# Performance work log

Measured on AMD Instinct MI355X. Metric: run time of the kernel, lower is better.

## Reference

```python
import jax, jax.numpy as jnp
import numpy as np

B, T1, T2, C, H, NIN = 4, 4096, 2048, 512, 8, 3
D = C // H  # head_dim = 64


def setup_inputs() -> dict:
    key = jax.random.key(0)
    ks = jax.random.split(key, 10)
    s = 0.02  # weight init scale
    return {
        "x": jax.random.normal(ks[0], (B, T1, C), jnp.float32),
        "y0": jax.random.normal(ks[1], (B, T2, C), jnp.float32),
        "y1": jax.random.normal(ks[2], (B, T2, C), jnp.float32),
        "y2": jax.random.normal(ks[3], (B, T2, C), jnp.float32),
        "Wq": jax.random.normal(ks[4], (C, C), jnp.float32) * s,
        "bq": jnp.zeros((C,), jnp.float32),
        "Wk": jax.random.normal(ks[5], (NIN, C, C), jnp.float32) * s,
        "bk": jnp.zeros((NIN, C), jnp.float32),
        "Wv": jax.random.normal(ks[6], (NIN, C, C), jnp.float32) * s,
        "bv": jnp.zeros((NIN, C), jnp.float32),
        "Wo": jax.random.normal(ks[7], (C, C), jnp.float32) * s,
        "bo": jnp.zeros((C,), jnp.float32),
    }


def _heads(t, n_head):
    b, n, c = t.shape
    return t.reshape(b, n, n_head, c // n_head).transpose(0, 2, 1, 3)  # [B,H,N,D]


def reference(x, y0, y1, y2, Wq, bq, Wk, bk, Wv, bv, Wo, bo):
    b, t1, c = x.shape
    q = jax.nn.softmax(_heads(x @ Wq.T + bq, H), axis=-1)  # [B,H,T1,D]
    out = q  # note: original initializes accumulator with q itself
    for i, y in enumerate((y0, y1, y2)):
        k = jax.nn.softmax(_heads(y @ Wk[i].T + bk[i], H), axis=-1)  # [B,H,T2,D]
        v = _heads(y @ Wv[i].T + bv[i], H)                            # [B,H,T2,D]
        k_sum = k.sum(axis=-2, keepdims=True)                         # [B,H,1,D]
        D_inv = 1.0 / ((q * k_sum).sum(axis=-1, keepdims=True) + 1e-8)  # [B,H,T1,1]
        context = jnp.einsum('bhnd,bhnv->bhdv', k, v)                 # [B,H,D,D]
        out = out + jnp.einsum('bhqd,bhdv->bhqv', q, context) * D_inv
    out = out.transpose(0, 2, 1, 3).reshape(b, t1, c)
    return out @ Wo.T + bo
```

## Files before the change

### kernel.cpp

```cpp
#include <hip/hip_runtime.h>
#include <stdint.h>

#define B_ 4
#define T1_ 4096
#define T2_ 2048
#define C_ 512
#define H_ 8
#define D_ 64
#define M1_ (B_*T1_)
#define M2_ (B_*T2_)

using f32x4 = __attribute__((ext_vector_type(4))) float;
using bf16x8 = __attribute__((ext_vector_type(8))) __bf16;
using us8 = __attribute__((ext_vector_type(8))) unsigned short;
using us4 = __attribute__((ext_vector_type(4))) unsigned short;

__device__ __forceinline__ unsigned short f2bf(float f){
  unsigned int u = __builtin_bit_cast(unsigned int, f);
  unsigned int r = (u + 0x7fffu + ((u >> 16) & 1u)) >> 16;
  return (unsigned short)r;
}
__device__ __forceinline__ float bf2f(unsigned short u){
  return __builtin_bit_cast(float, ((unsigned int)u) << 16);
}
__device__ __forceinline__ f32x4 mfma16(us8 a, us8 b, f32x4 c){
  return __builtin_amdgcn_mfma_f32_16x16x32_bf16(
      __builtin_bit_cast(bf16x8, a), __builtin_bit_cast(bf16x8, b), c, 0, 0, 0);
}
__device__ __forceinline__ us8 cvt8(f32x4 a, f32x4 b){
  us8 v;
  #pragma unroll
  for (int j = 0; j < 4; ++j){ v[j] = f2bf(a[j]); v[4+j] = f2bf(b[j]); }
  return v;
}

typedef const __attribute__((address_space(1))) unsigned int gu32;
typedef __attribute__((address_space(3))) unsigned int lu32;
__device__ __forceinline__ void gl_lds16(const void* g, void* l){
  __builtin_amdgcn_global_load_lds((gu32*)g, (lu32*)l, 16, 0, 0);
}

#define WAIT_VM(N) asm volatile("s_waitcnt vmcnt(" #N ")" ::: "memory")
#define WAIT_LGKM() asm volatile("s_waitcnt lgkmcnt(0)" ::: "memory")
#define RAW_BAR()  { __builtin_amdgcn_s_barrier(); __builtin_amdgcn_sched_barrier(0); }

__device__ __forceinline__ int swz(int row, int blk){ return blk ^ ((row >> 1) & 3); }

__global__ __launch_bounds__(256) void cvt_bf16_4(const float* __restrict__ p0, const float* __restrict__ p1,
                                                  const float* __restrict__ p2, const float* __restrict__ p3,
                                                  unsigned short* o0, unsigned short* o1,
                                                  unsigned short* o2, unsigned short* o3,
                                                  int n0, int n1, int n2, int n3){
  const float* in; unsigned short* out; int n4;
  switch (blockIdx.y){
    case 0: in = p0; out = o0; n4 = n0; break;
    case 1: in = p1; out = o1; n4 = n1; break;
    case 2: in = p2; out = o2; n4 = n2; break;
    default: in = p3; out = o3; n4 = n3; break;
  }
  int i = blockIdx.x * 256 + threadIdx.x;
  if (i >= n4) return;
  f32x4 v = ((const f32x4*)in)[i];
  us4 o;
  #pragma unroll
  for (int j = 0; j < 4; ++j) o[j] = f2bf(v[j]);
  ((us4*)out)[i] = o;
}

__device__ __forceinline__ void tile_write(unsigned short* tile, const f32x4 (&vals)[4][4],
                                           int wr, int wc, int lr, int lk){
  #pragma unroll
  for (int mt = 0; mt < 4; ++mt)
    #pragma unroll
    for (int nt = 0; nt < 4; ++nt)
      #pragma unroll
      for (int r = 0; r < 4; ++r){
        int row = wr*64 + mt*16 + lk*4 + r;
        int cb  = (wc*128 + nt*32 + lr*2) ^ ((row & 7) << 4);
        *(unsigned short*)((char*)tile + row*256 + cb) = f2bf(vals[mt][nt][r]);
      }
}
__device__ __forceinline__ void tile_write_T(unsigned short* tile, const f32x4 (&vals)[4][4],
                                             int wr, int wc, int lr, int lk){
  #pragma unroll
  for (int mt = 0; mt < 4; ++mt)
    #pragma unroll
    for (int nt = 0; nt < 4; ++nt)
      #pragma unroll
      for (int r = 0; r < 4; ++r){
        int n  = wr*64 + mt*16 + lk*4 + r;
        int ch = wc*64 + nt*16 + lr;
        int cb = (n*2) ^ ((ch & 7) << 4);
        *(unsigned short*)((char*)tile + ch*256 + cb) = f2bf(vals[mt][nt][r]);
      }
}
__device__ __forceinline__ void tile_flush(const unsigned short* tile, unsigned short* g,
                                           size_t row0, int col0, int ldg, int t){
  #pragma unroll
  for (int p = 0; p < 8; ++p){
    int row = p*16 + (t >> 4);
    int cb  = ((t & 15) * 16) ^ ((row & 7) << 4);
    us8 v = *(const us8*)((const char*)tile + row*256 + cb);
    *(us8*)(g + (row0 + row) * (size_t)ldg + col0 + (t & 15) * 8) = v;
  }
}

__global__ __launch_bounds__(256, 3) void proj(const float* __restrict__ xf,
                                               const float* __restrict__ y0f,
                                               const float* __restrict__ y1f,
                                               const float* __restrict__ y2f,
                                               const unsigned short* __restrict__ wqb,
                                               const unsigned short* __restrict__ wkb,
                                               const unsigned short* __restrict__ wvb,
                                               const float* __restrict__ bq,
                                               const float* __restrict__ bk,
                                               const float* __restrict__ bv,
                                               unsigned short* __restrict__ qb,
                                               unsigned short* __restrict__ kbT,
                                               unsigned short* __restrict__ vbT,
                                               float* __restrict__ ksum){
  __shared__ unsigned short smem[20480];
  const int hw = blockIdx.x;
  const int work = (hw & 7) * 256 + (hw >> 3);
  int seg, ii, m0, n0;
  const float* Af;
  const unsigned short* W;
  const float* bias;
  if (work < 512){
    seg = 0; ii = 0;
    m0 = (work >> 2) << 7; n0 = (work & 3) << 7;
    Af = xf; W = wqb; bias = bq;
  } else {
    int r = work - 512;
    int g = r >> 3, s = r & 7;
    ii = g >> 6; m0 = (g & 63) << 7;
    seg = (s < 4) ? 1 : 2;
    n0 = (s & 3) << 7;
    Af = (ii == 0) ? y0f : (ii == 1 ? y1f : y2f);
    W = (seg == 1 ? wkb : wvb) + (size_t)ii*C_*C_;
    bias = (seg == 1 ? bk : bv) + (size_t)ii*C_;
  }
  const int t = threadIdx.x;
  const int w = t >> 6, l = t & 63;
  const int wr = w >> 1, wc = w & 1;
  const int lr = l & 15, lk = l >> 4;
  const int row0 = t >> 2,          b0 = t & 3;
  const int row1 = (t + 256) >> 2,  b1 = t & 3;
  f32x4 acc[4][4] = {};
  f32x4 ar0[4], ar1[4];

#define LOADA(AR, TT) { \
    const float* ap0 = Af + (size_t)(m0+row0)*C_ + (TT)*32 + b0*8; \
    const float* ap1 = Af + (size_t)(m0+row1)*C_ + (TT)*32 + b1*8; \
    AR[0] = *(const f32x4*)ap0; AR[1] = *(const f32x4*)(ap0 + 4); \
    AR[2] = *(const f32x4*)ap1; AR[3] = *(const f32x4*)(ap1 + 4); }
#define DSWA(AR, BUF) { \
    *(us8*)&smem[(BUF)*4096 + row0*32 + swz(row0,b0)*8] = cvt8(AR[0], AR[1]); \
    *(us8*)&smem[(BUF)*4096 + row1*32 + swz(row1,b1)*8] = cvt8(AR[2], AR[3]); }
#define GLW(BUF, TT) { \
    int c=t, row=c>>2; \
    gl_lds16(W + (size_t)(n0+row)*C_ + (TT)*32 + swz(row,c&3)*8, &smem[8192+(BUF)*4096 + c*8]); \
    c=t+256; row=c>>2; \
    gl_lds16(W + (size_t)(n0+row)*C_ + (TT)*32 + swz(row,c&3)*8, &smem[8192+(BUF)*4096 + c*8]); }
#define PCOMP(S, WB) { \
    const unsigned short* sA = &smem[(S)*4096]; \
    const unsigned short* sW = &smem[8192 + (WB)*4096]; \
    us8 af[4], bfr[4]; \
    _Pragma("unroll") \
    for (int mt = 0; mt < 4; ++mt){ int R = wr*64 + mt*16 + lr; af[mt] = *(const us8*)&sA[R*32 + swz(R, lk)*8]; } \
    _Pragma("unroll") \
    for (int nt = 0; nt < 4; ++nt){ int R = wc*64 + nt*16 + lr; bfr[nt] = *(const us8*)&sW[R*32 + swz(R, lk)*8]; } \
    __builtin_amdgcn_s_setprio(1); \
    _Pragma("unroll") \
    for (int mt = 0; mt < 4; ++mt) \
      _Pragma("unroll") \
      for (int nt = 0; nt < 4; ++nt) \
        acc[mt][nt] = mfma16(af[mt], bfr[nt], acc[mt][nt]); \
    __builtin_amdgcn_s_setprio(0); }
#define PSTEP(T, AR, S) { \
    WAIT_VM(6); \
    DSWA(AR, S); \
    if ((T) + 2 < 16) { LOADA(AR, (T)+2); GLW(((T)+2)%3, (T)+2); } \
    WAIT_LGKM(); \
    RAW_BAR(); \
    PCOMP(S, (T)%3); }
#define PSTEPL(T, AR, S) { \
    WAIT_VM(0); \
    DSWA(AR, S); \
    WAIT_LGKM(); \
    RAW_BAR(); \
    PCOMP(S, (T)%3); }

  LOADA(ar0, 0); GLW(0, 0);
  LOADA(ar1, 1); GLW(1, 1);
  PSTEP(0,  ar0, 0) PSTEP(1,  ar1, 1) PSTEP(2,  ar0, 0) PSTEP(3,  ar1, 1)
  PSTEP(4,  ar0, 0) PSTEP(5,  ar1, 1) PSTEP(6,  ar0, 0) PSTEP(7,  ar1, 1)
  PSTEP(8,  ar0, 0) PSTEP(9,  ar1, 1) PSTEP(10, ar0, 0) PSTEP(11, ar1, 1)
  PSTEP(12, ar0, 0) PSTEP(13, ar1, 1) PSTEP(14, ar0, 0) PSTEPL(15, ar1, 1)
#undef LOADA
#undef DSWA
#undef GLW
#undef PCOMP
#undef PSTEP
#undef PSTEPL

  {
    float bc[4];
    #pragma unroll
    for (int nt = 0; nt < 4; ++nt) bc[nt] = bias[n0 + wc*64 + nt*16 + lr];
    #pragma unroll
    for (int mt = 0; mt < 4; ++mt)
      #pragma unroll
      for (int nt = 0; nt < 4; ++nt)
        #pragma unroll
        for (int r = 0; r < 4; ++r) acc[mt][nt][r] += bc[nt];
  }
  if (seg <= 1){
    #pragma unroll
    for (int mt = 0; mt < 4; ++mt)
      #pragma unroll
      for (int r = 0; r < 4; ++r){
        float m = fmaxf(fmaxf(acc[mt][0][r], acc[mt][1][r]), fmaxf(acc[mt][2][r], acc[mt][3][r]));
        #pragma unroll
        for (int s = 1; s < 16; s <<= 1) m = fmaxf(m, __shfl_xor(m, s, 64));
        float sum = 0.f;
        #pragma unroll
        for (int nt = 0; nt < 4; ++nt){
          float e = __expf(acc[mt][nt][r] - m);
          acc[mt][nt][r] = e; sum += e;
        }
        #pragma unroll
        for (int s = 1; s < 16; s <<= 1) sum += __shfl_xor(sum, s, 64);
        float inv = 1.0f / sum;
        #pragma unroll
        for (int nt = 0; nt < 4; ++nt) acc[mt][nt][r] *= inv;
      }
  }
  if (seg == 1){
    const int b = m0 >> 11;
    #pragma unroll
    for (int nt = 0; nt < 4; ++nt){
      float cs = 0.f;
      #pragma unroll
      for (int mt = 0; mt < 4; ++mt)
        #pragma unroll
        for (int r = 0; r < 4; ++r) cs += acc[mt][nt][r];
      cs += __shfl_xor(cs, 16, 64);
      cs += __shfl_xor(cs, 32, 64);
      if (lk == 0)
        atomicAdd(&ksum[((size_t)ii*B_ + b)*C_ + n0 + wc*64 + nt*16 + lr], cs);
    }
  }
  __syncthreads();
  if (seg == 0){
    tile_write(smem, acc, wr, wc, lr, lk);
    __syncthreads();
    tile_flush(smem, qb, m0, n0, C_, t);
  } else {
    tile_write_T(smem, acc, wr, wc, lr, lk);
    __syncthreads();
    const int b = m0 >> 11;
    const int n_base = m0 & 2047;
    unsigned short* gT = (seg == 1 ? kbT : vbT);
    tile_flush(smem, gT, ((size_t)ii*B_ + b)*C_ + n0, n_base, T2_, t);
  }
}

__global__ __launch_bounds__(256) void ctx_mfma(const unsigned short* __restrict__ kbT,
                                                const unsigned short* __restrict__ vbT,
                                                float* __restrict__ part){
  const int bh = blockIdx.x, kc = blockIdx.y, i = blockIdx.z;
  const int b = bh >> 3, h = bh & 7;
  const size_t rowbase = ((size_t)i*B_ + b)*C_ + h*64;
  const unsigned short* kT = kbT + rowbase*T2_;
  const unsigned short* vT = vbT + rowbase*T2_;
  const int t = threadIdx.x;
  const int w = t >> 6, l = t & 63;
  const int qr = w >> 1, qc = w & 1;
  const int lr = l & 15, lk = l >> 4;
  const int n00 = kc * 256;
  f32x4 acc[2][2] = {};
  #pragma unroll
  for (int it = 0; it < 8; ++it){
    const int k0 = n00 + it*32 + lk*8;
    us8 a0 = *(const us8*)(kT + (size_t)(qr*32 +      lr)*T2_ + k0);
    us8 a1 = *(const us8*)(kT + (size_t)(qr*32 + 16 + lr)*T2_ + k0);
    us8 b0 = *(const us8*)(vT + (size_t)(qc*32 +      lr)*T2_ + k0);
    us8 b1 = *(const us8*)(vT + (size_t)(qc*32 + 16 + lr)*T2_ + k0);
    acc[0][0] = mfma16(a0, b0, acc[0][0]);
    acc[0][1] = mfma16(a0, b1, acc[0][1]);
    acc[1][0] = mfma16(a1, b0, acc[1][0]);
    acc[1][1] = mfma16(a1, b1, acc[1][1]);
  }
  float* dst = part + (((size_t)i*8 + kc)*32 + bh)*4096;
  #pragma unroll
  for (int fa = 0; fa < 2; ++fa)
    #pragma unroll
    for (int fb = 0; fb < 2; ++fb){
      int d0 = qr*32 + fa*16 + lk*4;
      int e  = qc*32 + fb*16 + lr;
      *(f32x4*)(dst + e*64 + d0) = acc[fa][fb];
    }
}

__global__ __launch_bounds__(256) void ctx_reduce(const float* __restrict__ part,
                                                  unsigned short* __restrict__ ctxTb){
  const int bh = blockIdx.x, i = blockIdx.y, t = threadIdx.x;
  for (int idx = t; idx < 4096; idx += 256){
    float s = 0.f;
    #pragma unroll
    for (int kc = 0; kc < 8; ++kc)
      s += part[(((size_t)i*8 + kc)*32 + bh)*4096 + idx];
    ctxTb[((size_t)i*32 + bh)*4096 + idx] = f2bf(s);
  }
}

__global__ __launch_bounds__(256) void combine(const unsigned short* __restrict__ qb,
                                               const unsigned short* __restrict__ ctxTb,
                                               const float* __restrict__ ksum,
                                               unsigned short* __restrict__ omid){
  __shared__ unsigned short tile[128*128];
  const int hw = blockIdx.x;
  const int work = (hw & 7) * 64 + (hw >> 3);
  const int m0 = (work & 127) << 7, n0 = (work >> 7) << 7;
  const int t = threadIdx.x;
  const int w = t >> 6, l = t & 63;
  const int wr = w >> 1, wc = w & 1;
  const int lr = l & 15, lk = l >> 4;
  const int b = m0 >> 12;
  const int bh = b*8 + (n0 >> 6) + wc;
  #pragma unroll
  for (int p = 0; p < 8; ++p){
    int idx = p*256 + t;
    int row = idx >> 4, ch = idx & 15;
    gl_lds16(qb + (size_t)(m0+row)*C_ + n0 + (ch ^ (row & 7))*8, &tile[idx*8]);
  }
  WAIT_VM(0);
  __syncthreads();
  us8 afr[4][2];
  #pragma unroll
  for (int mt = 0; mt < 4; ++mt)
    #pragma unroll
    for (int kk = 0; kk < 2; ++kk){
      int row = wr*64 + mt*16 + lr;
      int ch = wc*8 + kk*4 + lk;
      afr[mt][kk] = *(const us8*)((const char*)tile + row*256 + ((ch ^ (row & 7)) << 4));
    }
  f32x4 acc[4][4];
  #pragma unroll
  for (int mt = 0; mt < 4; ++mt)
    #pragma unroll
    for (int nt = 0; nt < 4; ++nt)
      #pragma unroll
      for (int r = 0; r < 4; ++r){
        int row = wr*64 + mt*16 + lk*4 + r;
        int cbyte = wc*128 + nt*32 + lr*2;
        int ch = cbyte >> 4;
        unsigned short v = *(const unsigned short*)((const char*)tile + row*256 +
                            ((ch ^ (row & 7)) << 4) + (cbyte & 15));
        acc[mt][nt][r] = bf2f(v);
      }
  us8 bden[2];
  #pragma unroll
  for (int kk = 0; kk < 2; ++kk){
    us8 tmp = {};
    if (lr < 3){
      const float* kp = ksum + ((size_t)lr*B_ + b)*C_ + n0 + wc*64 + kk*32 + lk*8;
      f32x4 c0 = *(const f32x4*)kp;
      f32x4 c1 = *(const f32x4*)(kp + 4);
      #pragma unroll
      for (int j = 0; j < 4; ++j){ tmp[j] = f2bf(c0[j]); tmp[4+j] = f2bf(c1[j]); }
    }
    bden[kk] = tmp;
  }
  f32x4 den[4] = {};
  #pragma unroll
  for (int mt = 0; mt < 4; ++mt)
    #pragma unroll
    for (int kk = 0; kk < 2; ++kk)
      den[mt] = mfma16(afr[mt][kk], bden[kk], den[mt]);
  #pragma unroll 1
  for (int i = 0; i < 3; ++i){
    f32x4 dinv[4];
    #pragma unroll
    for (int mt = 0; mt < 4; ++mt)
      #pragma unroll
      for (int r = 0; r < 4; ++r)
        dinv[mt][r] = 1.0f / (__shfl(den[mt][r], (l & 48) | i, 64) + 1e-8f);
    #pragma unroll
    for (int nt = 0; nt < 4; ++nt){
      us8 bfr[2];
      #pragma unroll
      for (int kk = 0; kk < 2; ++kk)
        bfr[kk] = *(const us8*)(ctxTb + ((size_t)(i*32 + bh))*4096 + (nt*16 + lr)*64 + kk*32 + lk*8);
      f32x4 p[4] = {};
      #pragma unroll
      for (int mt = 0; mt < 4; ++mt)
        #pragma unroll
        for (int kk = 0; kk < 2; ++kk)
          p[mt] = mfma16(afr[mt][kk], bfr[kk], p[mt]);
      #pragma unroll
      for (int mt = 0; mt < 4; ++mt)
        #pragma unroll
        for (int r = 0; r < 4; ++r)
          acc[mt][nt][r] += p[mt][r] * dinv[mt][r];
    }
  }
  __syncthreads();
  tile_write(tile, acc, wr, wc, lr, lk);
  __syncthreads();
  tile_flush(tile, omid, m0, n0, C_, t);
}

__global__ __launch_bounds__(256, 3) void gemm_bt(const unsigned short* __restrict__ A,
                                                  const unsigned short* __restrict__ Bw,
                                                  const float* __restrict__ bias,
                                                  float* __restrict__ out){
  __shared__ unsigned short smem[3*2*4096];
  const int hw = blockIdx.x;
  const int work = (hw & 7) * 64 + (hw >> 3);
  const int m0 = ((work >> 2) & 127) << 7, n0 = (work & 3) << 7;
  const int t = threadIdx.x;
  const int w = t >> 6, l = t & 63;
  const int wr = w >> 1, wc = w & 1;
  const int lr = l & 15, lk = l >> 4;
  f32x4 acc[4][4] = {};

#define GSTAGE(BB, TT) { \
    int c = t, row = c >> 2; \
    gl_lds16(A  + (size_t)(m0+row)*C_ + (TT)*32 + swz(row, c & 3)*8, &smem[(BB)*8192 + c*8]); \
    gl_lds16(Bw + (size_t)(n0+row)*C_ + (TT)*32 + swz(row, c & 3)*8, &smem[(BB)*8192 + 4096 + c*8]); \
    c = t + 256; row = c >> 2; \
    gl_lds16(A  + (size_t)(m0+row)*C_ + (TT)*32 + swz(row, c & 3)*8, &smem[(BB)*8192 + c*8]); \
    gl_lds16(Bw + (size_t)(n0+row)*C_ + (TT)*32 + swz(row, c & 3)*8, &smem[(BB)*8192 + 4096 + c*8]); }
#define GCOMP(BB) { \
    const unsigned short* sA = &smem[(BB)*8192]; \
    const unsigned short* sB = &smem[(BB)*8192 + 4096]; \
    us8 af[4], bfr[4]; \
    _Pragma("unroll") \
    for (int mt = 0; mt < 4; ++mt){ int R = wr*64 + mt*16 + lr; af[mt] = *(const us8*)&sA[R*32 + swz(R, lk)*8]; } \
    _Pragma("unroll") \
    for (int nt = 0; nt < 4; ++nt){ int R = wc*64 + nt*16 + lr; bfr[nt] = *(const us8*)&sB[R*32 + swz(R, lk)*8]; } \
    __builtin_amdgcn_s_setprio(1); \
    _Pragma("unroll") \
    for (int mt = 0; mt < 4; ++mt) \
      _Pragma("unroll") \
      for (int nt = 0; nt < 4; ++nt) \
        acc[mt][nt] = mfma16(af[mt], bfr[nt], acc[mt][nt]); \
    __builtin_amdgcn_s_setprio(0); }
#define GSTEP(T, N) { \
    if ((T) + 2 < 16) GSTAGE(((T)+2)%3, (T)+2); \
    WAIT_VM(N); \
    RAW_BAR(); \
    GCOMP((T)%3); }

  GSTAGE(0, 0); GSTAGE(1, 1);
  GSTEP(0, 8)  GSTEP(1, 8)  GSTEP(2, 8)  GSTEP(3, 8)
  GSTEP(4, 8)  GSTEP(5, 8)  GSTEP(6, 8)  GSTEP(7, 8)
  GSTEP(8, 8)  GSTEP(9, 8)  GSTEP(10, 8) GSTEP(11, 8)
  GSTEP(12, 8) GSTEP(13, 8) GSTEP(14, 4) GSTEP(15, 0)
#undef GSTAGE
#undef GCOMP
#undef GSTEP

  #pragma unroll
  for (int mt = 0; mt < 4; ++mt)
    #pragma unroll
    for (int nt = 0; nt < 4; ++nt)
      #pragma unroll
      for (int r = 0; r < 4; ++r){
        int row = m0 + wr*64 + mt*16 + lk*4 + r;
        int col = n0 + wc*64 + nt*16 + lr;
        out[(size_t)row*C_ + col] = acc[mt][nt][r] + bias[col];
      }
}

extern "C" void kernel_launch(void* const* d_in, const int* in_sizes, int n_in,
                              void* d_out, int out_size, void* d_ws, size_t ws_size,
                              hipStream_t stream){
  const float* x  = (const float*)d_in[0];
  const float* y0 = (const float*)d_in[1];
  const float* y1 = (const float*)d_in[2];
  const float* y2 = (const float*)d_in[3];
  const float* Wq = (const float*)d_in[4];
  const float* bq = (const float*)d_in[5];
  const float* Wk = (const float*)d_in[6];
  const float* bk = (const float*)d_in[7];
  const float* Wv = (const float*)d_in[8];
  const float* bv = (const float*)d_in[9];
  const float* Wo = (const float*)d_in[10];
  const float* bo = (const float*)d_in[11];

  char* ws = (char*)d_ws;
  size_t off = 0;
  auto alloc = [&](size_t bytes)->char*{
    char* p = ws + off; off += (bytes + 1023) & ~((size_t)1023); return p;
  };
  unsigned short* wqb   = (unsigned short*)alloc((size_t)C_*C_*2);
  unsigned short* wkb   = (unsigned short*)alloc((size_t)3*C_*C_*2);
  unsigned short* wvb   = (unsigned short*)alloc((size_t)3*C_*C_*2);
  unsigned short* wob   = (unsigned short*)alloc((size_t)C_*C_*2);
  unsigned short* qb    = (unsigned short*)alloc((size_t)M1_*C_*2);
  unsigned short* kbT   = (unsigned short*)alloc((size_t)3*B_*C_*T2_*2);
  unsigned short* vbT   = (unsigned short*)alloc((size_t)3*B_*C_*T2_*2);
  float*          ksum  = (float*)alloc((size_t)3*B_*C_*4);
  float*          part  = (float*)alloc((size_t)3*8*32*4096*4);
  unsigned short* ctxTb = (unsigned short*)alloc((size_t)3*32*4096*2);
  unsigned short* omid  = (unsigned short*)alloc((size_t)M1_*C_*2);

  (void)hipMemsetAsync(ksum, 0, (size_t)3*B_*C_*4, stream);

  cvt_bf16_4<<<dim3(3*C_*C_/4/256, 4), 256, 0, stream>>>(
      Wq, Wk, Wv, Wo, wqb, wkb, wvb, wob,
      C_*C_/4, 3*C_*C_/4, 3*C_*C_/4, C_*C_/4);

  proj<<<2048, 256, 0, stream>>>(x, y0, y1, y2, wqb, wkb, wvb, bq, bk, bv, qb, kbT, vbT, ksum);
  ctx_mfma<<<dim3(32, 8, 3), 256, 0, stream>>>(kbT, vbT, part);
  ctx_reduce<<<dim3(32, 3), 256, 0, stream>>>(part, ctxTb);
  combine<<<512, 256, 0, stream>>>(qb, ctxTb, ksum, omid);
  gemm_bt<<<512, 256, 0, stream>>>(omid, wob, bo, (float*)d_out);
}
```

Before: 125.2 us.

## Triple-buffer A tile in proj GEMM and use one barrier per k-step

Restructures the projection GEMM main loop so the A operand (fp32 converted to bf16) is triple-buffered in LDS like W. Each step writes the next A tile and issues the next global loads, then runs the MFMAs on the current stage, with a single barrier at the end of the step instead of a barrier right before compute. The aim is to overlap the LDS stores and global loads with matrix math and to cut barrier stalls. It also replaces the manual bf16 rounding with the native __bf16 conversion. LDS use rises from 40 KB to 48 KB per block, which may affect the 3-blocks-per-CU occupancy target, and the vmcnt bookkeeping is delicate.

```diff
diff --git a/kernel.cpp b/kernel.cpp
--- a/kernel.cpp
+++ b/kernel.cpp
@@ -30,7 +30,10 @@
 __device__ __forceinline__ us8 cvt8(f32x4 a, f32x4 b){
   us8 v;
   #pragma unroll
-  for (int j = 0; j < 4; ++j){ v[j] = f2bf(a[j]); v[4+j] = f2bf(b[j]); }
+  for (int j = 0; j < 4; ++j){
+    v[j]   = __builtin_bit_cast(unsigned short, (__bf16)a[j]);
+    v[4+j] = __builtin_bit_cast(unsigned short, (__bf16)b[j]);
+  }
   return v;
 }
 
@@ -119,7 +122,7 @@
                                                unsigned short* __restrict__ kbT,
                                                unsigned short* __restrict__ vbT,
                                                float* __restrict__ ksum){
-  __shared__ unsigned short smem[20480];
+  __shared__ unsigned short smem[24576];
   const int hw = blockIdx.x;
   const int work = (hw & 7) * 256 + (hw >> 3);
   int seg, ii, m0, n0;
@@ -159,12 +162,12 @@
     *(us8*)&smem[(BUF)*4096 + row1*32 + swz(row1,b1)*8] = cvt8(AR[2], AR[3]); }
 #define GLW(BUF, TT) { \
     int c=t, row=c>>2; \
-    gl_lds16(W + (size_t)(n0+row)*C_ + (TT)*32 + swz(row,c&3)*8, &smem[8192+(BUF)*4096 + c*8]); \
+    gl_lds16(W + (size_t)(n0+row)*C_ + (TT)*32 + swz(row,c&3)*8, &smem[12288+(BUF)*4096 + c*8]); \
     c=t+256; row=c>>2; \
-    gl_lds16(W + (size_t)(n0+row)*C_ + (TT)*32 + swz(row,c&3)*8, &smem[8192+(BUF)*4096 + c*8]); }
+    gl_lds16(W + (size_t)(n0+row)*C_ + (TT)*32 + swz(row,c&3)*8, &smem[12288+(BUF)*4096 + c*8]); }
 #define PCOMP(S, WB) { \
     const unsigned short* sA = &smem[(S)*4096]; \
-    const unsigned short* sW = &smem[8192 + (WB)*4096]; \
+    const unsigned short* sW = &smem[12288 + (WB)*4096]; \
     us8 af[4], bfr[4]; \
     _Pragma("unroll") \
     for (int mt = 0; mt < 4; ++mt){ int R = wr*64 + mt*16 + lr; af[mt] = *(const us8*)&sA[R*32 + swz(R, lk)*8]; } \
@@ -177,32 +180,41 @@
       for (int nt = 0; nt < 4; ++nt) \
         acc[mt][nt] = mfma16(af[mt], bfr[nt], acc[mt][nt]); \
     __builtin_amdgcn_s_setprio(0); }
-#define PSTEP(T, AR, S) { \
+#define PSTEP(T, ARW, ARL) { \
+    WAIT_VM(2); \
+    DSWA(ARW, ((T)+1)%3); \
+    LOADA(ARL, (T)+2); \
+    GLW(((T)+2)%3, (T)+2); \
+    PCOMP((T)%3, (T)%3); \
+    WAIT_LGKM(); \
     WAIT_VM(6); \
-    DSWA(AR, S); \
-    if ((T) + 2 < 16) { LOADA(AR, (T)+2); GLW(((T)+2)%3, (T)+2); } \
-    WAIT_LGKM(); \
-    RAW_BAR(); \
-    PCOMP(S, (T)%3); }
-#define PSTEPL(T, AR, S) { \
-    WAIT_VM(0); \
-    DSWA(AR, S); \
-    WAIT_LGKM(); \
-    RAW_BAR(); \
-    PCOMP(S, (T)%3); }
+    RAW_BAR(); }
 
   LOADA(ar0, 0); GLW(0, 0);
   LOADA(ar1, 1); GLW(1, 1);
-  PSTEP(0,  ar0, 0) PSTEP(1,  ar1, 1) PSTEP(2,  ar0, 0) PSTEP(3,  ar1, 1)
-  PSTEP(4,  ar0, 0) PSTEP(5,  ar1, 1) PSTEP(6,  ar0, 0) PSTEP(7,  ar1, 1)
-  PSTEP(8,  ar0, 0) PSTEP(9,  ar1, 1) PSTEP(10, ar0, 0) PSTEP(11, ar1, 1)
-  PSTEP(12, ar0, 0) PSTEP(13, ar1, 1) PSTEP(14, ar0, 0) PSTEPL(15, ar1, 1)
+  WAIT_VM(8);
+  DSWA(ar0, 0);
+  WAIT_LGKM();
+  WAIT_VM(6);
+  RAW_BAR();
+  PSTEP(0,  ar1, ar0) PSTEP(1,  ar0, ar1) PSTEP(2,  ar1, ar0) PSTEP(3,  ar0, ar1)
+  PSTEP(4,  ar1, ar0) PSTEP(5,  ar0, ar1) PSTEP(6,  ar1, ar0) PSTEP(7,  ar0, ar1)
+  PSTEP(8,  ar1, ar0) PSTEP(9,  ar0, ar1) PSTEP(10, ar1, ar0) PSTEP(11, ar0, ar1)
+  PSTEP(12, ar1, ar0) PSTEP(13, ar0, ar1)
+  {
+    WAIT_VM(2);
+    DSWA(ar1, 0);
+    PCOMP(2, 2);
+    WAIT_LGKM();
+    WAIT_VM(0);
+    RAW_BAR();
+  }
+  PCOMP(0, 0);
 #undef LOADA
 #undef DSWA
 #undef GLW
 #undef PCOMP
 #undef PSTEP
-#undef PSTEPL
 
   {
     float bc[4];
```

Result: no change. 123.3 us (-1.6%).
